# Optimization experiments

Hardware: AMD Instinct MI355X
Metric: run time of the kernel (lower is better)

## Reference

```python
import jax, jax.numpy as jnp
import numpy as np

N = 100000      # num_nodes
E = 1600000     # num_edges
F_IN = 128      # node_feature_dim
D_IN = F_IN + 1 # +1 input_cards indicator
H = 128         # hidden dim (both layers)
NUM_CARDS = 110


def _xavier(key, shape):
    fan_out, fan_in = shape
    limit = np.sqrt(6.0 / (fan_in + fan_out))
    return jax.random.uniform(key, shape, jnp.float32, -limit, limit)


def setup_inputs() -> dict:
    key = jax.random.key(0)
    ks = jax.random.split(key, 12)
    x = jax.random.normal(ks[0], (N, F_IN), jnp.float32)
    edge_index = jax.random.randint(ks[1], (2, E), 0, N, jnp.int64)
    input_cards = jax.random.randint(ks[2], (N,), 0, 2, jnp.int32)
    # SAGEConv layer 1: lin_l (neighbors), lin_r (self), each [H, D_IN] + bias
    Wl1 = _xavier(ks[3], (H, D_IN)); bl1 = jnp.zeros((H,), jnp.float32)
    Wr1 = _xavier(ks[4], (H, D_IN)); br1 = jnp.zeros((H,), jnp.float32)
    # SAGEConv layer 2
    Wl2 = _xavier(ks[5], (H, H)); bl2 = jnp.zeros((H,), jnp.float32)
    Wr2 = _xavier(ks[6], (H, H)); br2 = jnp.zeros((H,), jnp.float32)
    # output layer: normal(0, 0.01)
    Wo = 0.01 * jax.random.normal(ks[7], (NUM_CARDS, H), jnp.float32)
    bo = jnp.zeros((NUM_CARDS,), jnp.float32)
    return {"x": x, "Wl1": Wl1, "bl1": bl1, "Wr1": Wr1, "br1": br1,
            "Wl2": Wl2, "bl2": bl2, "Wr2": Wr2, "br2": br2,
            "Wo": Wo, "bo": bo,
            "edge_index": edge_index, "input_cards": input_cards}


def _sage_conv_mean(h, src, dst, deg_inv, Wl, bl, Wr, br):
    # mean-aggregate source-node features at destination nodes
    summed = jax.ops.segment_sum(h[src], dst, num_segments=N)  # [N, d]
    mean = summed * deg_inv[:, None]
    return mean @ Wl.T + bl + h @ Wr.T + br


def reference(x, Wl1, bl1, Wr1, br1, Wl2, bl2, Wr2, br2, Wo, bo,
              edge_index, input_cards):
    src, dst = edge_index[0], edge_index[1]
    deg = jax.ops.segment_sum(jnp.ones((E,), jnp.float32), dst, num_segments=N)
    deg_inv = jnp.where(deg > 0, 1.0 / jnp.maximum(deg, 1.0), 0.0)
    h = jnp.concatenate([x, input_cards.astype(jnp.float32)[:, None]], axis=1)  # [N, D_IN]
    h = jax.nn.relu(_sage_conv_mean(h, src, dst, deg_inv, Wl1, bl1, Wr1, br1))
    h = jax.nn.relu(_sage_conv_mean(h, src, dst, deg_inv, Wl2, bl2, Wr2, br2))
    logits = h @ Wo.T + bo  # [N, NUM_CARDS]
    return logits
```

## Files before the change

kernel.cpp:

```cpp
#include <hip/hip_runtime.h>
#include <hip/hip_bf16.h>

#define N_NODES 100000
#define N_EDGES 1600000
#define HDIM    128
#define KCH     4
#define NUM_CARDS 110
#define NTILES  (N_NODES / 16)
#define GEMM_BLOCKS 1024

#define NB      196
#define MAXB    10240
#define PT      4096
#define PEPT    16

typedef __attribute__((ext_vector_type(8))) short bfrag;
typedef __attribute__((ext_vector_type(4))) float ffrag;
typedef __attribute__((ext_vector_type(2))) float f32x2;

__device__ inline unsigned short f2bf(float f) {
    __hip_bfloat16 h = __float2bfloat16(f);
    unsigned short u; __builtin_memcpy(&u, &h, 2); return u;
}
__device__ inline float bf_lo(unsigned int u) {
    unsigned int v = u << 16; float f; __builtin_memcpy(&f, &v, 4); return f;
}
__device__ inline float bf_hi(unsigned int u) {
    unsigned int v = u & 0xffff0000u; float f; __builtin_memcpy(&f, &v, 4); return f;
}


__global__ __launch_bounds__(256) void k_partition(
    const int* __restrict__ src, const int* __restrict__ dst,
    int* __restrict__ bucket_cursor, unsigned int* __restrict__ part) {
    __shared__ int hist[NB];
    __shared__ int hcur[NB];
    const int t = threadIdx.x;
    const int base = blockIdx.x * PT;
    for (int i = t; i < NB; i += 256) hist[i] = 0;
    __syncthreads();
#pragma unroll
    for (int i = 0; i < PEPT; i++) {
        int e = base + i * 256 + t;
        if (e < N_EDGES) atomicAdd(&hist[dst[e] >> 9], 1);
    }
    __syncthreads();
    for (int b = t; b < NB; b += 256) {
        int h = hist[b];
        hcur[b] = h ? atomicAdd(&bucket_cursor[b], h) : 0;
    }
    __syncthreads();
#pragma unroll
    for (int i = 0; i < PEPT; i++) {
        int e = base + i * 256 + t;
        if (e < N_EDGES) {
            int d = dst[e];
            int b = d >> 9;
            int r = atomicAdd(&hcur[b], 1);
            if (r < MAXB)
                part[(size_t)b * MAXB + r] =
                    ((unsigned int)(d & 511) << 17) | (unsigned int)src[e];
        }
    }
}

__global__ __launch_bounds__(256) void k_bucket(
    const unsigned int* __restrict__ part, const int* __restrict__ bucket_cursor,
    int* __restrict__ row_off, int* __restrict__ deg, float* __restrict__ deg_inv,
    int* __restrict__ csr_src) {
    __shared__ int degl[512];
    __shared__ int offl[512];
    __shared__ int curl[512];
    __shared__ int stmp[256];
    const int t = threadIdx.x;
    const int b = blockIdx.x;
    const int n0 = b << 9;
    const int nb = min(512, N_NODES - n0);
    const int cnt = min(bucket_cursor[b], MAXB);
    const int row0 = b * MAXB;
    const unsigned int* pb = &part[(size_t)b * MAXB];

    degl[t] = 0; degl[t + 256] = 0;
    __syncthreads();
    for (int i = t; i < cnt; i += 256)
        atomicAdd(&degl[pb[i] >> 17], 1);
    __syncthreads();
    const int a0 = degl[2 * t], a1 = degl[2 * t + 1];
    stmp[t] = a0 + a1;
    __syncthreads();
    for (int off = 1; off < 256; off <<= 1) {
        int x = (t >= off) ? stmp[t - off] : 0;
        __syncthreads();
        stmp[t] += x;
        __syncthreads();
    }
    const int excl = stmp[t] - (a0 + a1);
    offl[2 * t] = excl;          curl[2 * t] = excl;
    offl[2 * t + 1] = excl + a0; curl[2 * t + 1] = excl + a0;
    __syncthreads();
    for (int i = t; i < nb; i += 256) {
        int n = n0 + i;
        int d = degl[i];
        row_off[n] = row0 + offl[i];
        deg[n] = d;
        deg_inv[n] = (d > 0) ? 1.0f / (float)d : 0.0f;
    }
    for (int i = t; i < cnt; i += 256) {
        unsigned int pk = pb[i];
        int r = atomicAdd(&curl[pk >> 17], 1);
        csr_src[row0 + r] = (int)(pk & 0x1FFFFu);
    }
}


__global__ void k_prep_w(const float* __restrict__ Wl1, const float* __restrict__ Wr1,
                         const float* __restrict__ bl1, const float* __restrict__ br1,
                         const float* __restrict__ Wl2, const float* __restrict__ Wr2,
                         const float* __restrict__ bl2, const float* __restrict__ br2,
                         const float* __restrict__ Wo,  const float* __restrict__ bo,
                         unsigned short* __restrict__ W1, unsigned short* __restrict__ W2,
                         unsigned short* __restrict__ Wob,
                         float* __restrict__ bias1, float* __restrict__ bias2,
                         float* __restrict__ biaso, float* __restrict__ wcard1) {
    const int j = blockIdx.x;
    const int k = threadIdx.x;
    const float* s1 = (j < 128) ? &Wl1[(size_t)j * 129] : &Wr1[(size_t)(j - 128) * 129];
    W1[(size_t)j * HDIM + k] = f2bf(s1[k]);
    const float* s2 = (j < 128) ? &Wl2[(size_t)j * HDIM] : &Wr2[(size_t)(j - 128) * HDIM];
    W2[(size_t)j * HDIM + k] = f2bf(s2[k]);
    if (j < 112)
        Wob[(size_t)j * HDIM + k] = (j < NUM_CARDS) ? f2bf(Wo[(size_t)j * HDIM + k])
                                                    : (unsigned short)0;
    if (k == 0) {
        wcard1[j] = s1[HDIM];
        bias1[j] = (j < 128) ? 0.f : (bl1[j - 128] + br1[j - 128]);
        bias2[j] = (j < 128) ? 0.f : (bl2[j - 128] + br2[j - 128]);
        if (j < 112) biaso[j] = (j < NUM_CARDS) ? bo[j] : 0.f;
    }
}


__global__ __launch_bounds__(256) void k_gemm_dual(
    const unsigned short* __restrict__ Ab, const float* __restrict__ Af,
    const int* __restrict__ cards,
    const unsigned short* __restrict__ W,
    const float* __restrict__ bias, const float* __restrict__ wcard,
    unsigned char* __restrict__ Gq, unsigned short* __restrict__ Rb,
    int layer1) {
    const int wave = threadIdx.x >> 6;
    const int lane = threadIdx.x & 63;
    const int m16 = lane & 15;
    const int quad = lane >> 4;
    const int u0 = wave * 4;
    const bool isG = (wave < 2);

    bfrag wf[4][KCH];
    float bs[4][4], wc[4][4];
#pragma unroll
    for (int u = 0; u < 4; u++) {
        const int j = (u0 + u) * 16 + m16;
#pragma unroll
        for (int c = 0; c < KCH; c++)
            wf[u][c] = *(const bfrag*)&W[(size_t)j * HDIM + c * 32 + quad * 8];
#pragma unroll
        for (int r = 0; r < 4; r++) {
            const int jj = (u0 + u) * 16 + quad * 4 + r;
            bs[u][r] = bias[jj];
            wc[u][r] = layer1 ? wcard[jj] : 0.f;
        }
    }

    for (int tile = blockIdx.x; tile < NTILES; tile += GEMM_BLOCKS) {
        const int node = tile * 16 + m16;
        bfrag hf[KCH];
        float cv = 0.f;
        if (layer1) {
#pragma unroll
            for (int c = 0; c < KCH; c++) {
                const float4 p0 = *(const float4*)&Af[(size_t)node * HDIM + c * 32 + quad * 8];
                const float4 p1 = *(const float4*)&Af[(size_t)node * HDIM + c * 32 + quad * 8 + 4];
                bfrag h;
                h[0] = (short)f2bf(p0.x); h[1] = (short)f2bf(p0.y);
                h[2] = (short)f2bf(p0.z); h[3] = (short)f2bf(p0.w);
                h[4] = (short)f2bf(p1.x); h[5] = (short)f2bf(p1.y);
                h[6] = (short)f2bf(p1.z); h[7] = (short)f2bf(p1.w);
                hf[c] = h;
            }
            cv = (float)cards[node];
        } else {
#pragma unroll
            for (int c = 0; c < KCH; c++)
                hf[c] = *(const bfrag*)&Ab[(size_t)node * HDIM + c * 32 + quad * 8];
        }
#pragma unroll
        for (int u = 0; u < 4; u++) {
            ffrag acc = {0.f, 0.f, 0.f, 0.f};
#pragma unroll
            for (int c = 0; c < KCH; c++)
                acc = __builtin_amdgcn_mfma_f32_16x16x32_bf16(wf[u][c], hf[c], acc, 0, 0, 0);
            float v[4];
#pragma unroll
            for (int r = 0; r < 4; r++)
                v[r] = acc[r] + bs[u][r] + cv * wc[u][r];
            if (isG) {
                int pk = __builtin_amdgcn_cvt_pk_fp8_f32(v[0], v[1], 0, false);
                pk = __builtin_amdgcn_cvt_pk_fp8_f32(v[2], v[3], pk, true);
                *(unsigned int*)&Gq[(size_t)node * HDIM + (u0 + u) * 16 + quad * 4] =
                    (unsigned int)pk;
            } else {
                unsigned short o[4];
#pragma unroll
                for (int r = 0; r < 4; r++) o[r] = f2bf(v[r]);
                uint2 p = {(unsigned int)o[0] | ((unsigned int)o[1] << 16),
                           (unsigned int)o[2] | ((unsigned int)o[3] << 16)};
                *(uint2*)&Rb[(size_t)node * HDIM + (u0 + u - 8) * 16 + quad * 4] = p;
            }
        }
    }
}


__global__ __launch_bounds__(256) void k_agg(
    const unsigned char* __restrict__ Gq, const unsigned short* __restrict__ Rb,
    const int* __restrict__ row_off, const int* __restrict__ deg,
    const float* __restrict__ deg_inv, const int* __restrict__ csr_src,
    unsigned short* __restrict__ outH) {
    const int wave = threadIdx.x >> 6;
    const int lane = threadIdx.x & 63;
    const int n = blockIdx.x * 4 + wave;
    const int g = lane >> 3;
    const int l = lane & 7;
    const int start = row_off[n];
    const int d = deg[n];
    const int fo = l * 16;

    int myoff = 0;
    if (lane < d) myoff = csr_src[start + lane] * HDIM;

    uint4 rv0 = {0u, 0u, 0u, 0u}, rv1 = {0u, 0u, 0u, 0u};
    if (g == 0) {
        rv0 = *(const uint4*)&Rb[(size_t)n * HDIM + l * 16];
        rv1 = *(const uint4*)&Rb[(size_t)n * HDIM + l * 16 + 8];
    }

    f32x2 acc2[8];
#pragma unroll
    for (int i = 0; i < 8; i++) acc2[i] = (f32x2){0.f, 0.f};

    const int iters = (d + 7) >> 3;

    uint4 cur = {0u, 0u, 0u, 0u};
    {
        const int off0 = __shfl(myoff, g, 64);
        if (g < d) cur = *(const uint4*)&Gq[(size_t)(unsigned)off0 + fo];
    }
    for (int i = 1; i < iters; i++) {
        const int jj = i * 8 + g;
        const int offn = __shfl(myoff, jj & 63, 64);
        uint4 nxt = {0u, 0u, 0u, 0u};
        if (jj < d) {
            const int o = (jj < 64) ? offn : csr_src[start + jj] * HDIM;
            nxt = *(const uint4*)&Gq[(size_t)(unsigned)o + fo];
        }
        acc2[0] += __builtin_amdgcn_cvt_pk_f32_fp8((int)cur.x, false);
        acc2[1] += __builtin_amdgcn_cvt_pk_f32_fp8((int)cur.x, true);
        acc2[2] += __builtin_amdgcn_cvt_pk_f32_fp8((int)cur.y, false);
        acc2[3] += __builtin_amdgcn_cvt_pk_f32_fp8((int)cur.y, true);
        acc2[4] += __builtin_amdgcn_cvt_pk_f32_fp8((int)cur.z, false);
        acc2[5] += __builtin_amdgcn_cvt_pk_f32_fp8((int)cur.z, true);
        acc2[6] += __builtin_amdgcn_cvt_pk_f32_fp8((int)cur.w, false);
        acc2[7] += __builtin_amdgcn_cvt_pk_f32_fp8((int)cur.w, true);
        cur = nxt;
    }
    acc2[0] += __builtin_amdgcn_cvt_pk_f32_fp8((int)cur.x, false);
    acc2[1] += __builtin_amdgcn_cvt_pk_f32_fp8((int)cur.x, true);
    acc2[2] += __builtin_amdgcn_cvt_pk_f32_fp8((int)cur.y, false);
    acc2[3] += __builtin_amdgcn_cvt_pk_f32_fp8((int)cur.y, true);
    acc2[4] += __builtin_amdgcn_cvt_pk_f32_fp8((int)cur.z, false);
    acc2[5] += __builtin_amdgcn_cvt_pk_f32_fp8((int)cur.z, true);
    acc2[6] += __builtin_amdgcn_cvt_pk_f32_fp8((int)cur.w, false);
    acc2[7] += __builtin_amdgcn_cvt_pk_f32_fp8((int)cur.w, true);

#pragma unroll
    for (int i = 0; i < 8; i++) {
        f32x2 v = acc2[i];
        f32x2 t;
        t.x = __shfl_xor(v.x, 8, 64);  t.y = __shfl_xor(v.y, 8, 64);  v += t;
        t.x = __shfl_xor(v.x, 16, 64); t.y = __shfl_xor(v.y, 16, 64); v += t;
        t.x = __shfl_xor(v.x, 32, 64); t.y = __shfl_xor(v.y, 32, 64); v += t;
        acc2[i] = v;
    }
    if (g == 0) {
        const float di = deg_inv[n];
        const float r[16] = {bf_lo(rv0.x), bf_hi(rv0.x), bf_lo(rv0.y), bf_hi(rv0.y),
                             bf_lo(rv0.z), bf_hi(rv0.z), bf_lo(rv0.w), bf_hi(rv0.w),
                             bf_lo(rv1.x), bf_hi(rv1.x), bf_lo(rv1.y), bf_hi(rv1.y),
                             bf_lo(rv1.z), bf_hi(rv1.z), bf_lo(rv1.w), bf_hi(rv1.w)};
        unsigned short o[16];
#pragma unroll
        for (int i = 0; i < 8; i++) {
            o[2 * i]     = f2bf(fmaxf(acc2[i].x * di + r[2 * i], 0.f));
            o[2 * i + 1] = f2bf(fmaxf(acc2[i].y * di + r[2 * i + 1], 0.f));
        }
        uint4 p0, p1;
        p0.x = (unsigned int)o[0] | ((unsigned int)o[1] << 16);
        p0.y = (unsigned int)o[2] | ((unsigned int)o[3] << 16);
        p0.z = (unsigned int)o[4] | ((unsigned int)o[5] << 16);
        p0.w = (unsigned int)o[6] | ((unsigned int)o[7] << 16);
        p1.x = (unsigned int)o[8] | ((unsigned int)o[9] << 16);
        p1.y = (unsigned int)o[10] | ((unsigned int)o[11] << 16);
        p1.z = (unsigned int)o[12] | ((unsigned int)o[13] << 16);
        p1.w = (unsigned int)o[14] | ((unsigned int)o[15] << 16);
        *(uint4*)&outH[(size_t)n * HDIM + l * 16] = p0;
        *(uint4*)&outH[(size_t)n * HDIM + l * 16 + 8] = p1;
    }
}


__global__ __launch_bounds__(256) void k_gemm_logits(
    const unsigned short* __restrict__ A, const unsigned short* __restrict__ W,
    const float* __restrict__ bias, float* __restrict__ out) {
    const int wave = threadIdx.x >> 6;
    const int lane = threadIdx.x & 63;
    const int m16 = lane & 15;
    const int quad = lane >> 4;
    const int u0 = wave * 2;

    bfrag wf[2][KCH];
    float bsj[2];
#pragma unroll
    for (int u = 0; u < 2; u++) {
        const int unit = u0 + u;
        const int j = (unit < 7 ? unit : 0) * 16 + m16;
#pragma unroll
        for (int c = 0; c < KCH; c++)
            wf[u][c] = *(const bfrag*)&W[(size_t)j * HDIM + c * 32 + quad * 8];
        bsj[u] = bias[j];
    }

    for (int tile = blockIdx.x; tile < NTILES; tile += GEMM_BLOCKS) {
        const int nodef = tile * 16 + m16;
        bfrag hf[KCH];
#pragma unroll
        for (int c = 0; c < KCH; c++)
            hf[c] = *(const bfrag*)&A[(size_t)nodef * HDIM + c * 32 + quad * 8];
#pragma unroll
        for (int u = 0; u < 2; u++) {
            const int unit = u0 + u;
            if (unit >= 7) break;
            ffrag acc = {0.f, 0.f, 0.f, 0.f};
#pragma unroll
            for (int c = 0; c < KCH; c++)
                acc = __builtin_amdgcn_mfma_f32_16x16x32_bf16(hf[c], wf[u][c], acc, 0, 0, 0);
            const int j = unit * 16 + m16;
            if (j < NUM_CARDS) {
#pragma unroll
                for (int r = 0; r < 4; r++) {
                    const int node = tile * 16 + quad * 4 + r;
                    out[(size_t)node * NUM_CARDS + j] = acc[r] + bsj[u];
                }
            }
        }
    }
}


static inline size_t align_up(size_t x, size_t a) { return (x + a - 1) & ~(a - 1); }

extern "C" void kernel_launch(void* const* d_in, const int* in_sizes, int n_in,
                              void* d_out, int out_size, void* d_ws, size_t ws_size,
                              hipStream_t stream) {
    const float* x   = (const float*)d_in[0];
    const float* Wl1 = (const float*)d_in[1];
    const float* bl1 = (const float*)d_in[2];
    const float* Wr1 = (const float*)d_in[3];
    const float* br1 = (const float*)d_in[4];
    const float* Wl2 = (const float*)d_in[5];
    const float* bl2 = (const float*)d_in[6];
    const float* Wr2 = (const float*)d_in[7];
    const float* br2 = (const float*)d_in[8];
    const float* Wo  = (const float*)d_in[9];
    const float* bo  = (const float*)d_in[10];
    const int* edge  = (const int*)d_in[11];
    const int* cards = (const int*)d_in[12];
    float* logits = (float*)d_out;

    const int* e_src = edge;
    const int* e_dst = edge + N_EDGES;

    char* w = (char*)d_ws;
    size_t off = 0;
    int* bucket_cursor = (int*)(w + off); off = align_up(off + 256 * 4, 512);
    unsigned int* part = (unsigned int*)(w + off); off = align_up(off + (size_t)NB * MAXB * 4, 512);
    int* row_off = (int*)(w + off); off = align_up(off + N_NODES * 4, 512);
    int* deg_i   = (int*)(w + off); off = align_up(off + N_NODES * 4, 512);
    float* dinv  = (float*)(w + off); off = align_up(off + N_NODES * 4, 512);
    int* csr_src = (int*)(w + off); off = align_up(off + (size_t)NB * MAXB * 4, 512);
    unsigned char*  Gq   = (unsigned char*)(w + off);  off = align_up(off + (size_t)N_NODES * HDIM, 512);
    unsigned short* Rb   = (unsigned short*)(w + off); off = align_up(off + (size_t)N_NODES * HDIM * 2, 512);
    unsigned short* bufH = (unsigned short*)(w + off); off = align_up(off + (size_t)N_NODES * HDIM * 2, 512);
    unsigned short* W1   = (unsigned short*)(w + off); off = align_up(off + 256 * HDIM * 2, 512);
    unsigned short* W2   = (unsigned short*)(w + off); off = align_up(off + 256 * HDIM * 2, 512);
    unsigned short* Wob  = (unsigned short*)(w + off); off = align_up(off + 112 * HDIM * 2, 512);
    float* bias1  = (float*)(w + off); off = align_up(off + 256 * 4, 512);
    float* bias2  = (float*)(w + off); off = align_up(off + 256 * 4, 512);
    float* biaso  = (float*)(w + off); off = align_up(off + 112 * 4, 512);
    float* wcard1 = (float*)(w + off); off = align_up(off + 256 * 4, 512);
    (void)ws_size; (void)n_in; (void)in_sizes; (void)out_size;

    hipMemsetAsync(bucket_cursor, 0, 256 * 4, stream);
    k_prep_w<<<256, 128, 0, stream>>>(Wl1, Wr1, bl1, br1, Wl2, Wr2, bl2, br2, Wo, bo,
                                      W1, W2, Wob, bias1, bias2, biaso, wcard1);

    const int PBLK = (N_EDGES + PT - 1) / PT;
    k_partition<<<PBLK, 256, 0, stream>>>(e_src, e_dst, bucket_cursor, part);
    k_bucket<<<NB, 256, 0, stream>>>(part, bucket_cursor,
                                     row_off, deg_i, dinv, csr_src);

    k_gemm_dual<<<GEMM_BLOCKS, 256, 0, stream>>>(nullptr, x, cards, W1, bias1, wcard1, Gq, Rb, 1);
    k_agg<<<N_NODES / 4, 256, 0, stream>>>(Gq, Rb, row_off, deg_i, dinv, csr_src, bufH);
    k_gemm_dual<<<GEMM_BLOCKS, 256, 0, stream>>>(bufH, nullptr, nullptr, W2, bias2, wcard1, Gq, Rb, 0);
    k_agg<<<N_NODES / 4, 256, 0, stream>>>(Gq, Rb, row_off, deg_i, dinv, csr_src, bufH);
    k_gemm_logits<<<GEMM_BLOCKS, 256, 0, stream>>>(bufH, Wob, biaso, logits);
}
```

Measured before the change: 366.2 us.

## Assign eight nodes per wave in aggregation, one 8-lane group per node

```diff
diff --git a/kernel.cpp b/kernel.cpp
--- a/kernel.cpp
+++ b/kernel.cpp
@@ -227,93 +227,81 @@
     unsigned short* __restrict__ outH) {
     const int wave = threadIdx.x >> 6;
     const int lane = threadIdx.x & 63;
-    const int n = blockIdx.x * 4 + wave;
     const int g = lane >> 3;
     const int l = lane & 7;
+    const int n = (blockIdx.x * 4 + wave) * 8 + g;
     const int start = row_off[n];
     const int d = deg[n];
+    const float di = deg_inv[n];
     const int fo = l * 16;
 
-    int myoff = 0;
-    if (lane < d) myoff = csr_src[start + lane] * HDIM;
-
-    uint4 rv0 = {0u, 0u, 0u, 0u}, rv1 = {0u, 0u, 0u, 0u};
-    if (g == 0) {
-        rv0 = *(const uint4*)&Rb[(size_t)n * HDIM + l * 16];
-        rv1 = *(const uint4*)&Rb[(size_t)n * HDIM + l * 16 + 8];
-    }
+    int dmax = d;
+    dmax = max(dmax, __shfl_xor(dmax, 8, 64));
+    dmax = max(dmax, __shfl_xor(dmax, 16, 64));
+    dmax = max(dmax, __shfl_xor(dmax, 32, 64));
+
+    const uint4 rv0 = *(const uint4*)&Rb[(size_t)n * HDIM + fo];
+    const uint4 rv1 = *(const uint4*)&Rb[(size_t)n * HDIM + fo + 8];
 
     f32x2 acc2[8];
 #pragma unroll
     for (int i = 0; i < 8; i++) acc2[i] = (f32x2){0.f, 0.f};
 
-    const int iters = (d + 7) >> 3;
+    int idxA = (l < d) ? csr_src[start + l] * HDIM : 0;
+    int idxB = (8 + l < d) ? csr_src[start + 8 + l] * HDIM : 0;
 
     uint4 cur = {0u, 0u, 0u, 0u};
     {
-        const int off0 = __shfl(myoff, g, 64);
-        if (g < d) cur = *(const uint4*)&Gq[(size_t)(unsigned)off0 + fo];
-    }
-    for (int i = 1; i < iters; i++) {
-        const int jj = i * 8 + g;
-        const int offn = __shfl(myoff, jj & 63, 64);
+        const int off0 = __shfl(idxA, g << 3, 64);
+        if (0 < d) cur = *(const uint4*)&Gq[(size_t)(unsigned)off0 + fo];
+    }
+#define ACC16(Cv)                                                        \
+    acc2[0] += __builtin_amdgcn_cvt_pk_f32_fp8((int)(Cv).x, false);      \
+    acc2[1] += __builtin_amdgcn_cvt_pk_f32_fp8((int)(Cv).x, true);       \
+    acc2[2] += __builtin_amdgcn_cvt_pk_f32_fp8((int)(Cv).y, false);      \
+    acc2[3] += __builtin_amdgcn_cvt_pk_f32_fp8((int)(Cv).y, true);       \
+    acc2[4] += __builtin_amdgcn_cvt_pk_f32_fp8((int)(Cv).z, false);      \
+    acc2[5] += __builtin_amdgcn_cvt_pk_f32_fp8((int)(Cv).z, true);       \
+    acc2[6] += __builtin_amdgcn_cvt_pk_f32_fp8((int)(Cv).w, false);      \
+    acc2[7] += __builtin_amdgcn_cvt_pk_f32_fp8((int)(Cv).w, true);
+
+    for (int i = 1; i < dmax; i++) {
+        const int sl = i & 7;
+        if (sl == 0) {
+            idxA = idxB;
+            const int j = i + 8 + l;
+            idxB = (j < d) ? csr_src[start + j] * HDIM : 0;
+        }
+        const int offn = __shfl(idxA, (g << 3) | sl, 64);
         uint4 nxt = {0u, 0u, 0u, 0u};
-        if (jj < d) {
-            const int o = (jj < 64) ? offn : csr_src[start + jj] * HDIM;
-            nxt = *(const uint4*)&Gq[(size_t)(unsigned)o + fo];
-        }
-        acc2[0] += __builtin_amdgcn_cvt_pk_f32_fp8((int)cur.x, false);
-        acc2[1] += __builtin_amdgcn_cvt_pk_f32_fp8((int)cur.x, true);
-        acc2[2] += __builtin_amdgcn_cvt_pk_f32_fp8((int)cur.y, false);
-        acc2[3] += __builtin_amdgcn_cvt_pk_f32_fp8((int)cur.y, true);
-        acc2[4] += __builtin_amdgcn_cvt_pk_f32_fp8((int)cur.z, false);
-        acc2[5] += __builtin_amdgcn_cvt_pk_f32_fp8((int)cur.z, true);
-        acc2[6] += __builtin_amdgcn_cvt_pk_f32_fp8((int)cur.w, false);
-        acc2[7] += __builtin_amdgcn_cvt_pk_f32_fp8((int)cur.w, true);
+        if (i < d) nxt = *(const uint4*)&Gq[(size_t)(unsigned)offn + fo];
+        ACC16(cur);
         cur = nxt;
     }
-    acc2[0] += __builtin_amdgcn_cvt_pk_f32_fp8((int)cur.x, false);
-    acc2[1] += __builtin_amdgcn_cvt_pk_f32_fp8((int)cur.x, true);
-    acc2[2] += __builtin_amdgcn_cvt_pk_f32_fp8((int)cur.y, false);
-    acc2[3] += __builtin_amdgcn_cvt_pk_f32_fp8((int)cur.y, true);
-    acc2[4] += __builtin_amdgcn_cvt_pk_f32_fp8((int)cur.z, false);
-    acc2[5] += __builtin_amdgcn_cvt_pk_f32_fp8((int)cur.z, true);
-    acc2[6] += __builtin_amdgcn_cvt_pk_f32_fp8((int)cur.w, false);
-    acc2[7] += __builtin_amdgcn_cvt_pk_f32_fp8((int)cur.w, true);
-
+    ACC16(cur);
+#undef ACC16
+
+    const float r[16] = {bf_lo(rv0.x), bf_hi(rv0.x), bf_lo(rv0.y), bf_hi(rv0.y),
+                         bf_lo(rv0.z), bf_hi(rv0.z), bf_lo(rv0.w), bf_hi(rv0.w),
+                         bf_lo(rv1.x), bf_hi(rv1.x), bf_lo(rv1.y), bf_hi(rv1.y),
+                         bf_lo(rv1.z), bf_hi(rv1.z), bf_lo(rv1.w), bf_hi(rv1.w)};
+    unsigned short o[16];
 #pragma unroll
     for (int i = 0; i < 8; i++) {
-        f32x2 v = acc2[i];
-        f32x2 t;
-        t.x = __shfl_xor(v.x, 8, 64);  t.y = __shfl_xor(v.y, 8, 64);  v += t;
-        t.x = __shfl_xor(v.x, 16, 64); t.y = __shfl_xor(v.y, 16, 64); v += t;
-        t.x = __shfl_xor(v.x, 32, 64); t.y = __shfl_xor(v.y, 32, 64); v += t;
-        acc2[i] = v;
-    }
-    if (g == 0) {
-        const float di = deg_inv[n];
-        const float r[16] = {bf_lo(rv0.x), bf_hi(rv0.x), bf_lo(rv0.y), bf_hi(rv0.y),
-                             bf_lo(rv0.z), bf_hi(rv0.z), bf_lo(rv0.w), bf_hi(rv0.w),
-                             bf_lo(rv1.x), bf_hi(rv1.x), bf_lo(rv1.y), bf_hi(rv1.y),
-                             bf_lo(rv1.z), bf_hi(rv1.z), bf_lo(rv1.w), bf_hi(rv1.w)};
-        unsigned short o[16];
-#pragma unroll
-        for (int i = 0; i < 8; i++) {
-            o[2 * i]     = f2bf(fmaxf(acc2[i].x * di + r[2 * i], 0.f));
-            o[2 * i + 1] = f2bf(fmaxf(acc2[i].y * di + r[2 * i + 1], 0.f));
-        }
-        uint4 p0, p1;
-        p0.x = (unsigned int)o[0] | ((unsigned int)o[1] << 16);
-        p0.y = (unsigned int)o[2] | ((unsigned int)o[3] << 16);
-        p0.z = (unsigned int)o[4] | ((unsigned int)o[5] << 16);
-        p0.w = (unsigned int)o[6] | ((unsigned int)o[7] << 16);
-        p1.x = (unsigned int)o[8] | ((unsigned int)o[9] << 16);
-        p1.y = (unsigned int)o[10] | ((unsigned int)o[11] << 16);
-        p1.z = (unsigned int)o[12] | ((unsigned int)o[13] << 16);
-        p1.w = (unsigned int)o[14] | ((unsigned int)o[15] << 16);
-        *(uint4*)&outH[(size_t)n * HDIM + l * 16] = p0;
-        *(uint4*)&outH[(size_t)n * HDIM + l * 16 + 8] = p1;
-    }
+        o[2 * i]     = f2bf(fmaxf(acc2[i].x * di + r[2 * i], 0.f));
+        o[2 * i + 1] = f2bf(fmaxf(acc2[i].y * di + r[2 * i + 1], 0.f));
+    }
+    uint4 p0, p1;
+    p0.x = (unsigned int)o[0] | ((unsigned int)o[1] << 16);
+    p0.y = (unsigned int)o[2] | ((unsigned int)o[3] << 16);
+    p0.z = (unsigned int)o[4] | ((unsigned int)o[5] << 16);
+    p0.w = (unsigned int)o[6] | ((unsigned int)o[7] << 16);
+    p1.x = (unsigned int)o[8] | ((unsigned int)o[9] << 16);
+    p1.y = (unsigned int)o[10] | ((unsigned int)o[11] << 16);
+    p1.z = (unsigned int)o[12] | ((unsigned int)o[13] << 16);
+    p1.w = (unsigned int)o[14] | ((unsigned int)o[15] << 16);
+    *(uint4*)&outH[(size_t)n * HDIM + fo] = p0;
+    *(uint4*)&outH[(size_t)n * HDIM + fo + 8] = p1;
 }
 
 
@@ -418,8 +406,8 @@
                                      row_off, deg_i, dinv, csr_src);
 
     k_gemm_dual<<<GEMM_BLOCKS, 256, 0, stream>>>(nullptr, x, cards, W1, bias1, wcard1, Gq, Rb, 1);
-    k_agg<<<N_NODES / 4, 256, 0, stream>>>(Gq, Rb, row_off, deg_i, dinv, csr_src, bufH);
+    k_agg<<<N_NODES / 32, 256, 0, stream>>>(Gq, Rb, row_off, deg_i, dinv, csr_src, bufH);
     k_gemm_dual<<<GEMM_BLOCKS, 256, 0, stream>>>(bufH, nullptr, nullptr, W2, bias2, wcard1, Gq, Rb, 0);
-    k_agg<<<N_NODES / 4, 256, 0, stream>>>(Gq, Rb, row_off, deg_i, dinv, csr_src, bufH);
+    k_agg<<<N_NODES / 32, 256, 0, stream>>>(Gq, Rb, row_off, deg_i, dinv, csr_src, bufH);
     k_gemm_logits<<<GEMM_BLOCKS, 256, 0, stream>>>(bufH, Wob, biaso, logits);
 }
```

Result: faster. 330.7 us (-9.7%).
